# Performance work log

Measured on AMD Instinct MI355X. Metric: run time of the kernel, lower is better.

## Reference

```python
import jax, jax.numpy as jnp
import numpy as np

B, J, HID, INTER, NL = 4096, 16, 128, 64, 4
NEG = -9.0e15
EDGES = [(0,1),(1,2),(2,3),(0,4),(4,5),(5,6),(0,7),(7,8),(8,9),(8,10),(10,11),(11,12),(8,13),(13,14),(14,15)]
GROUPED = [0,7,1,4,2,5,3,6,8,10,9,13,11,14,12,15]  # flattened nodes_group


def _adjacency_nonzeros():
    A = np.zeros((J, J), np.float32)
    for i, j in EDGES:
        A[i, j] = 1.0
        A[j, i] = 1.0
    A += np.eye(J, dtype=np.float32)
    rows, cols = np.nonzero(A)  # row-major, matches torch adj[mask] = e fill order
    return rows.astype(np.int32), cols.astype(np.int32)


def setup_inputs() -> dict:
    key = jax.random.key(0)
    ks = iter(jax.random.split(key, 64))
    rn = lambda shape, s: jax.random.normal(next(ks), shape, jnp.float32) * s
    rows, cols = _adjacency_nonzeros()
    nnz = rows.shape[0]  # 46
    inp = dict(
        x=jax.random.normal(next(ks), (B, J, 2), jnp.float32),
        # input SemGraphConv (2 -> HID) + its BatchNorm
        gc_in_W=rn((2, 2, HID), 0.7), gc_in_e=1.0 + rn((nnz,), 0.3), gc_in_b=rn((HID,), 0.05),
        bn_in_g=1.0 + rn((HID,), 0.05), bn_in_b=rn((HID,), 0.05),
        # 4 residual blocks x 2 graph convs (HID -> HID)
        W_res=rn((2 * NL, 2, HID, HID), 0.08), e_res=1.0 + rn((2 * NL, nnz), 0.3),
        b_res=rn((2 * NL, HID), 0.05),
        bng_res=1.0 + rn((2 * NL, HID), 0.05), bnb_res=rn((2 * NL, HID), 0.05),
        # 5 GraphNonLocal blocks (1 after input + 1 per residual block)
        nl_g_w=rn((NL + 1, INTER, HID), 0.08), nl_g_b=rn((NL + 1, INTER), 0.05),
        nl_t_w=rn((NL + 1, INTER, HID), 0.08), nl_t_b=rn((NL + 1, INTER), 0.05),
        nl_p_w=rn((NL + 1, INTER, HID), 0.08), nl_p_b=rn((NL + 1, INTER), 0.05),
        nl_cp_w=rn((NL + 1, 2 * INTER), 0.08),  # concat_project 1x1 conv, no bias
        nl_W_w=rn((NL + 1, HID, INTER), 0.08), nl_W_b=rn((NL + 1, HID), 0.05),
        nl_bn_g=1.0 + rn((NL + 1, HID), 0.05), nl_bn_b=rn((NL + 1, HID), 0.05),
        # output SemGraphConv (HID -> 3)
        gc_out_W=rn((2, HID, 3), 0.08), gc_out_e=1.0 + rn((nnz,), 0.3), gc_out_b=rn((3,), 0.05),
        # integer constants
        mask_rows=jnp.asarray(rows), mask_cols=jnp.asarray(cols),
        grouped_order=jnp.asarray(GROUPED, jnp.int32),
        restored_order=jnp.asarray(np.argsort(GROUPED), jnp.int32),
    )
    return inp


def reference(x, gc_in_W, gc_in_e, gc_in_b, bn_in_g, bn_in_b,
              W_res, e_res, b_res, bng_res, bnb_res,
              nl_g_w, nl_g_b, nl_t_w, nl_t_b, nl_p_w, nl_p_b,
              nl_cp_w, nl_W_w, nl_W_b, nl_bn_g, nl_bn_b,
              gc_out_W, gc_out_e, gc_out_b,
              mask_rows, mask_cols, grouped_order, restored_order):
    eye = jnp.eye(J, dtype=x.dtype)

    def gconv(h, W, e, b):
        # h: [B, J, F]
        h0 = jnp.einsum('bjf,fo->bjo', h, W[0])
        h1 = jnp.einsum('bjf,fo->bjo', h, W[1])
        logits = jnp.full((J, J), NEG, h.dtype).at[mask_rows, mask_cols].set(e)
        adj = jax.nn.softmax(logits, axis=1)
        diag = jnp.diagonal(adj)                     # adj*I picks diagonal scaling
        off = adj * (1.0 - eye)
        return diag[None, :, None] * h0 + jnp.einsum('ij,bjo->bio', off, h1) + b

    def bn(h, g, bta, axes):
        # training-mode BatchNorm (biased variance), per-channel
        m = h.mean(axes, keepdims=True)
        v = h.var(axes, keepdims=True)
        return (h - m) * jax.lax.rsqrt(v + 1e-5) * g + bta

    def graph_conv(h, W, e, b, gm, gb):
        h = gconv(h, W, e, b)
        h = bn(h, gm[None, None, :], gb[None, None, :], (0, 1))
        return jax.nn.relu(h)

    def nonlocal_block(h, i):
        xo = h[:, grouped_order]          # [B, J, C] regroup joints
        xc = xo.transpose(0, 2, 1)        # [B, C, J]
        conv = lambda w, bb: jnp.einsum('oc,bcj->boj', w, xc) + bb[None, :, None]
        pool = lambda t: t.reshape(B, INTER, J // 2, 2).max(-1)   # MaxPool1d(k=2)
        gx = pool(conv(nl_g_w[i], nl_g_b[i]))                     # [B, I, J/2]
        th = conv(nl_t_w[i], nl_t_b[i])                           # [B, I, J]
        ph = pool(conv(nl_p_w[i], nl_p_b[i]))                     # [B, I, J/2]
        wt, wp = nl_cp_w[i][:INTER], nl_cp_w[i][INTER:]
        # concat_project 1x1 conv over concat(theta,phi) decomposes into a sum
        f = jax.nn.relu(jnp.einsum('bch,c->bh', th, wt)[:, :, None]
                        + jnp.einsum('bcw,c->bw', ph, wp)[:, None, :])  # [B, J, J/2]
        f = f / (J // 2)
        y = jnp.einsum('bhw,bcw->bch', f, gx)                     # [B, I, J]
        Wy = jnp.einsum('oc,bch->boh', nl_W_w[i], y) + nl_W_b[i][None, :, None]
        Wy = bn(Wy, nl_bn_g[i][None, :, None], nl_bn_b[i][None, :, None], (0, 2))
        z = Wy + xc
        return z.transpose(0, 2, 1)[:, restored_order]

    out = graph_conv(x, gc_in_W, gc_in_e, gc_in_b, bn_in_g, bn_in_b)
    out = nonlocal_block(out, 0)
    for i in range(NL):
        res = out
        out = graph_conv(out, W_res[2 * i], e_res[2 * i], b_res[2 * i], bng_res[2 * i], bnb_res[2 * i])
        out = graph_conv(out, W_res[2 * i + 1], e_res[2 * i + 1], b_res[2 * i + 1], bng_res[2 * i + 1], bnb_res[2 * i + 1])
        out = res + out
        out = nonlocal_block(out, i + 1)
    return gconv(out, gc_out_W, gc_out_e, gc_out_b)  # [B, J, 3]
```

## Files before the change

kernel.cpp:

```cpp
#include <hip/hip_runtime.h>

#define B 4096
#define J 16
#define HID 128
#define INTER 64
#define NLAYERS 4
#define NEGV -9000000000000000.0f
#define ELEMS ((size_t)B*16*128)
#define NREP 16
#define SLOT 4096

typedef __attribute__((ext_vector_type(8))) short short8;
typedef __attribute__((ext_vector_type(4))) float f32x4;

static __device__ __forceinline__ unsigned short f2bf(float x) {
    unsigned u = __float_as_uint(x);
    unsigned r = u + 0x7fffu + ((u >> 16) & 1u);
    return (unsigned short)(r >> 16);
}
static __device__ __forceinline__ void splitbf(float x, unsigned short& h, unsigned short& l) {
    h = f2bf(x);
    float hf = __uint_as_float((unsigned)h << 16);
    l = f2bf(x - hf);
}
static __device__ __forceinline__ void splitbf4(float4 v, uint2& hh, uint2& ll) {
    unsigned short h0,l0,h1,l1,h2,l2,h3,l3;
    splitbf(v.x,h0,l0); splitbf(v.y,h1,l1); splitbf(v.z,h2,l2); splitbf(v.w,h3,l3);
    hh = make_uint2((unsigned)h0 | ((unsigned)h1<<16), (unsigned)h2 | ((unsigned)h3<<16));
    ll = make_uint2((unsigned)l0 | ((unsigned)l1<<16), (unsigned)l2 | ((unsigned)l3<<16));
}
static __device__ __forceinline__ f32x4 mfma16(short8 a, short8 b, f32x4 c) {
    return __builtin_amdgcn_mfma_f32_16x16x32_bf16(a, b, c, 0, 0, 0);
}
static __device__ __forceinline__ f32x4 mfma_split(short8 ah, short8 al,
                                                   short8 bh, short8 bl, f32x4 acc) {
    acc = mfma16(ah, bh, acc);
    acc = mfma16(ah, bl, acc);
    acc = mfma16(al, bh, acc);
    return acc;
}
static __device__ __forceinline__ float bfpair(unsigned short h, unsigned short l) {
    return __uint_as_float((unsigned)h << 16) + __uint_as_float((unsigned)l << 16);
}

__global__ void adj_kernel(const float* __restrict__ e_in,
                           const float* __restrict__ e_res,
                           const float* __restrict__ e_out,
                           const int* __restrict__ rows,
                           const int* __restrict__ cols, int nnz,
                           float* __restrict__ off_all,
                           float* __restrict__ diag_all) {
    int m = blockIdx.x;
    int i = threadIdx.x;
    const float* e = (m == 0) ? e_in : (m <= 8) ? e_res + (size_t)(m - 1) * nnz : e_out;
    float l[16];
    for (int j = 0; j < 16; j++) l[j] = NEGV;
    for (int k = 0; k < nnz; k++)
        if (rows[k] == i) l[cols[k]] = e[k];
    float mx = l[0];
    for (int j = 1; j < 16; j++) mx = fmaxf(mx, l[j]);
    float ex[16], s = 0.f;
    for (int j = 0; j < 16; j++) { ex[j] = expf(l[j] - mx); s += ex[j]; }
    float inv = 1.f / s;
    for (int j = 0; j < 16; j++) {
        float a = ex[j] * inv;
        if (j == i) { diag_all[m * 16 + i] = a; a = 0.f; }
        off_all[m * 256 + i * 16 + j] = a;
    }
}

#define WB_N   262144
#define NLW_N  122880
#define NLWW_N 40960
__global__ void prep_w_kernel(const float* __restrict__ W_res,
                              const float* __restrict__ g_w, const float* __restrict__ t_w,
                              const float* __restrict__ p_w, const float* __restrict__ W_w,
                              unsigned short* __restrict__ Wbh, unsigned short* __restrict__ Wbl,
                              unsigned short* __restrict__ nlwh, unsigned short* __restrict__ nlwl,
                              unsigned short* __restrict__ nlWh, unsigned short* __restrict__ nlWl) {
    int i = blockIdx.x * 256 + threadIdx.x;
    unsigned short h, l;
    if (i < WB_N) {
        int lay = i >> 15, rem = i & 32767, n = rem >> 8, k = rem & 255;
        int d = k >> 7, f = k & 127;
        splitbf(W_res[(((lay << 1) | d) * 128 + f) * 128 + n], h, l);
        Wbh[i] = h; Wbl[i] = l;
    } else if (i < WB_N + NLW_N) {
        int j = i - WB_N;
        int lay = j / 24576, r2 = j % 24576;
        int conv = r2 >> 13, oc = r2 & 8191;
        const float* src = conv == 0 ? g_w : conv == 1 ? t_w : p_w;
        splitbf(src[lay * 8192 + oc], h, l);
        nlwh[j] = h; nlwl[j] = l;
    } else if (i < WB_N + NLW_N + NLWW_N) {
        int j = i - WB_N - NLW_N;
        splitbf(W_w[j], h, l);
        nlWh[j] = h; nlWl[j] = l;
    }
}

__global__ void prep_vt_kernel(const float* __restrict__ t_w, const float* __restrict__ t_b,
                               const float* __restrict__ cp_w,
                               float* __restrict__ vt, float* __restrict__ ct) {
    int l = blockIdx.x, c = threadIdx.x;
    float s = 0.f;
    for (int c2 = 0; c2 < 64; c2++)
        s += cp_w[l * 128 + c2] * t_w[(l * 64 + c2) * 128 + c];
    vt[l * 128 + c] = s;
    if (c == 0) {
        float s2 = 0.f;
        for (int c2 = 0; c2 < 64; c2++) s2 += cp_w[l * 128 + c2] * t_b[l * 64 + c2];
        ct[l] = s2;
    }
}

__global__ __launch_bounds__(256) void gconv_in_kernel(
        const float* __restrict__ x, const float* __restrict__ W,
        const float* __restrict__ bias, const float* __restrict__ off,
        const float* __restrict__ diag, float* __restrict__ out,
        float* __restrict__ stats_out) {
    __shared__ float xs[16][2];
    __shared__ float gs[16][2];
    __shared__ float red[512];
    int b = blockIdx.x, t = threadIdx.x;
    if (t < 32) xs[t >> 1][t & 1] = x[b * 32 + t];
    __syncthreads();
    if (t < 32) {
        int i = t >> 1, f = t & 1;
        float g = 0.f;
        #pragma unroll
        for (int j = 0; j < 16; j++) g += off[i * 16 + j] * xs[j][f];
        gs[i][f] = g;
    }
    __syncthreads();
    int o = t & 127;
    float w00 = W[o], w01 = W[128 + o], w10 = W[256 + o], w11 = W[384 + o], bo = bias[o];
    float s = 0.f, q = 0.f;
    for (int idx = t; idx < 2048; idx += 256) {
        int i = idx >> 7;
        float v = diag[i] * (xs[i][0] * w00 + xs[i][1] * w01)
                + gs[i][0] * w10 + gs[i][1] * w11 + bo;
        out[(size_t)b * 2048 + idx] = v;
        s += v; q += v * v;
    }
    red[t] = s; red[256 + t] = q;
    __syncthreads();
    float* so = stats_out + (b & (NREP - 1)) * 256;
    if (t < 128) {
        atomicAdd(&so[t], red[t] + red[t + 128]);
        atomicAdd(&so[128 + t], red[256 + t] + red[256 + t + 128]);
    }
}

__global__ __launch_bounds__(256) void gconv_mfma_kernel(
        const float* src, const float* wy,
        const float* __restrict__ stats_in,
        const float* __restrict__ bn_g, const float* __restrict__ bn_b,
        const int* __restrict__ restored, float* zdst,
        const unsigned short* __restrict__ Wbh,
        const unsigned short* __restrict__ Wbl,
        const float* __restrict__ bias,
        const float* __restrict__ off, const float* __restrict__ diag,
        float* dst, float* __restrict__ stats_out) {
    __shared__ float hraw[16][132];
    __shared__ __align__(16) unsigned short ksh[16][264];
    __shared__ __align__(16) unsigned short ksl[16][264];
    __shared__ float offs[256];
    __shared__ float diags[16];
    int t = threadIdx.x;
    offs[t] = off[t];
    if (t < 16) diags[t] = diag[t];
    float* hrawf = &hraw[0][0];
    {
        float ssum = 0.f;
        #pragma unroll
        for (int rr = 0; rr < NREP; rr++) ssum += stats_in[rr * 256 + t];
        hrawf[t] = ssum;
    }
    int c4 = (4 * t) & 127;
    int r0 = t >> 5;
    int ro0 = 0, ro1 = 0;
    if (wy) { ro0 = restored[r0]; ro1 = restored[r0 + 8]; }
    int b0 = blockIdx.x;
    const float4* src4 = (const float4*)src;
    const float4* wy4  = (const float4*)wy;
    float4 sv0 = src4[(size_t)b0 * 512 + t];
    float4 sv1 = src4[(size_t)b0 * 512 + 256 + t];
    float4 wv0 = make_float4(0,0,0,0), wv1 = make_float4(0,0,0,0);
    if (wy) {
        wv0 = wy4[(size_t)b0 * 512 + ro0 * 32 + (c4 >> 2)];
        wv1 = wy4[(size_t)b0 * 512 + ro1 * 32 + (c4 >> 2)];
    }
    __syncthreads();
    float4 m4, sc4, bb4;
    {
        const float K = 1.f / 65536.f;
        float4 g4 = *(const float4*)&bn_g[c4];
        bb4 = *(const float4*)&bn_b[c4];
        float m0 = hrawf[c4]     * K, m1 = hrawf[c4 + 1] * K;
        float m2 = hrawf[c4 + 2] * K, m3 = hrawf[c4 + 3] * K;
        float i0 = rsqrtf(hrawf[128 + c4]     * K - m0 * m0 + 1e-5f);
        float i1 = rsqrtf(hrawf[128 + c4 + 1] * K - m1 * m1 + 1e-5f);
        float i2 = rsqrtf(hrawf[128 + c4 + 2] * K - m2 * m2 + 1e-5f);
        float i3 = rsqrtf(hrawf[128 + c4 + 3] * K - m3 * m3 + 1e-5f);
        m4 = make_float4(m0, m1, m2, m3);
        sc4 = make_float4(i0 * g4.x, i1 * g4.y, i2 * g4.z, i3 * g4.w);
    }
    __syncthreads();
    int wv_ = t >> 6, lane = t & 63;
    int mn = lane & 15, kq = (lane >> 4) << 3, qr = (lane >> 4) << 2;

    for (int s = 0; s < 2; s++) {
        int bb_ = blockIdx.x + s * 2048;
        {
            float4 v = sv0;
            if (wy) {
                v.x += (wv0.x - m4.x) * sc4.x + bb4.x;
                v.y += (wv0.y - m4.y) * sc4.y + bb4.y;
                v.z += (wv0.z - m4.z) * sc4.z + bb4.z;
                v.w += (wv0.w - m4.w) * sc4.w + bb4.w;
                ((float4*)zdst)[(size_t)bb_ * 512 + t] = v;
            } else {
                v.x = fmaxf((v.x - m4.x) * sc4.x + bb4.x, 0.f);
                v.y = fmaxf((v.y - m4.y) * sc4.y + bb4.y, 0.f);
                v.z = fmaxf((v.z - m4.z) * sc4.z + bb4.z, 0.f);
                v.w = fmaxf((v.w - m4.w) * sc4.w + bb4.w, 0.f);
            }
            *(float4*)&hraw[r0][c4] = v;
            v = sv1;
            if (wy) {
                v.x += (wv1.x - m4.x) * sc4.x + bb4.x;
                v.y += (wv1.y - m4.y) * sc4.y + bb4.y;
                v.z += (wv1.z - m4.z) * sc4.z + bb4.z;
                v.w += (wv1.w - m4.w) * sc4.w + bb4.w;
                ((float4*)zdst)[(size_t)bb_ * 512 + 256 + t] = v;
            } else {
                v.x = fmaxf((v.x - m4.x) * sc4.x + bb4.x, 0.f);
                v.y = fmaxf((v.y - m4.y) * sc4.y + bb4.y, 0.f);
                v.z = fmaxf((v.z - m4.z) * sc4.z + bb4.z, 0.f);
                v.w = fmaxf((v.w - m4.w) * sc4.w + bb4.w, 0.f);
            }
            *(float4*)&hraw[r0 + 8][c4] = v;
        }
        if (s == 0) {
            int b1 = blockIdx.x + 2048;
            sv0 = src4[(size_t)b1 * 512 + t];
            sv1 = src4[(size_t)b1 * 512 + 256 + t];
            if (wy) {
                wv0 = wy4[(size_t)b1 * 512 + ro0 * 32 + (c4 >> 2)];
                wv1 = wy4[(size_t)b1 * 512 + ro1 * 32 + (c4 >> 2)];
            }
        }
        __syncthreads();
        for (int u = t; u < 512; u += 256) {
            int i = u >> 5, f4 = (u & 31) << 2;
            float4 hv = *(const float4*)&hraw[i][f4];
            float4 g = make_float4(0.f, 0.f, 0.f, 0.f);
            #pragma unroll
            for (int j = 0; j < 16; j++) {
                float w = offs[i * 16 + j];
                float4 hj = *(const float4*)&hraw[j][f4];
                g.x += w * hj.x; g.y += w * hj.y; g.z += w * hj.z; g.w += w * hj.w;
            }
            float d = diags[i];
            uint2 hh, ll;
            splitbf4(make_float4(d * hv.x, d * hv.y, d * hv.z, d * hv.w), hh, ll);
            *(uint2*)&ksh[i][f4] = hh;
            *(uint2*)&ksl[i][f4] = ll;
            splitbf4(g, hh, ll);
            *(uint2*)&ksh[i][128 + f4] = hh;
            *(uint2*)&ksl[i][128 + f4] = ll;
        }
        __syncthreads();
        int n0 = wv_ << 5;
        f32x4 acc0 = {0.f, 0.f, 0.f, 0.f}, acc1 = {0.f, 0.f, 0.f, 0.f};
        const unsigned short* wh0 = Wbh + (size_t)(n0 + mn) * 256 + kq;
        const unsigned short* wl0 = Wbl + (size_t)(n0 + mn) * 256 + kq;
        #pragma unroll
        for (int k = 0; k < 8; k++) {
            int k0 = k << 5;
            short8 ah = *(const short8*)&ksh[mn][k0 + kq];
            short8 al = *(const short8*)&ksl[mn][k0 + kq];
            acc0 = mfma_split(ah, al, *(const short8*)(wh0 + k0), *(const short8*)(wl0 + k0), acc0);
            acc1 = mfma_split(ah, al, *(const short8*)(wh0 + 4096 + k0), *(const short8*)(wl0 + 4096 + k0), acc1);
        }
        float bias0 = bias[n0 + mn], bias1 = bias[n0 + 16 + mn];
        float s0 = 0.f, q0 = 0.f, s1 = 0.f, q1 = 0.f;
        #pragma unroll
        for (int r = 0; r < 4; r++) {
            int row = qr + r;
            float v0 = acc0[r] + bias0;
            float v1 = acc1[r] + bias1;
            dst[(size_t)bb_ * 2048 + row * 128 + n0 + mn] = v0;
            dst[(size_t)bb_ * 2048 + row * 128 + n0 + 16 + mn] = v1;
            s0 += v0; q0 += v0 * v0; s1 += v1; q1 += v1 * v1;
        }
        s0 += __shfl_xor(s0, 16); s0 += __shfl_xor(s0, 32);
        q0 += __shfl_xor(q0, 16); q0 += __shfl_xor(q0, 32);
        s1 += __shfl_xor(s1, 16); s1 += __shfl_xor(s1, 32);
        q1 += __shfl_xor(q1, 16); q1 += __shfl_xor(q1, 32);
        float* so = stats_out + (bb_ & (NREP - 1)) * 256;
        if (lane < 16) {
            atomicAdd(&so[n0 + mn], s0);
            atomicAdd(&so[128 + n0 + mn], q0);
            atomicAdd(&so[n0 + 16 + mn], s1);
            atomicAdd(&so[128 + n0 + 16 + mn], q1);
        }
        if (s == 0) __syncthreads();
    }
}

#define CG(conv, o, j) cgbuf[((conv) * 64 + (o)) * 17 + (j)]
#define WYL(o, j)      cgbuf[(o) * 17 + (j)]
__global__ __launch_bounds__(512, 8) void nl_a_kernel(
        const float* tsrc, const float* __restrict__ stats_in,
        const float* __restrict__ bn_g, const float* __restrict__ bn_b,
        const float* res,
        const unsigned short* __restrict__ nlwh,
        const unsigned short* __restrict__ nlwl,
        const float* __restrict__ g_b, const float* __restrict__ p_b,
        const float* __restrict__ cpw,
        const float* __restrict__ vt, const float* __restrict__ ctp,
        const unsigned short* __restrict__ nlWh,
        const unsigned short* __restrict__ nlWl,
        const float* __restrict__ W_b,
        const int* __restrict__ restored,
        float* hdst, float* wydst, float* __restrict__ wst) {
    __shared__ __align__(16) unsigned short xch[16][136];
    __shared__ __align__(16) unsigned short xcl[16][136];
    __shared__ float cgbuf[2176];
    __shared__ float gx[64][9];
    __shared__ float tv[16], pv[8];
    __shared__ float vtl[128];
    __shared__ __align__(16) float bnm[128], bnsc[128], bnbb[128];
    __shared__ __align__(16) unsigned short ybh[16][72];
    __shared__ __align__(16) unsigned short ybl[16][72];
    __shared__ float redS[512], redQ[512];
    int t = threadIdx.x, b = blockIdx.x;
    const float4* tsrc4 = (const float4*)tsrc;
    float4 sv = tsrc4[(size_t)b * 512 + t];
    float4 rv = make_float4(0.f, 0.f, 0.f, 0.f);
    if (res) rv = ((const float4*)res)[(size_t)b * 512 + t];
    if (t < 256) {
        float ssum = 0.f;
        #pragma unroll
        for (int rr = 0; rr < NREP; rr++) ssum += stats_in[rr * 256 + t];
        redS[t] = ssum;
    }
    if (t < 128) vtl[t] = vt[t];
    int c4 = (4 * t) & 127;
    int r0 = t >> 5;
    int rg = restored[r0];
    __syncthreads();
    if (t < 128) {
        const float K = 1.f / 65536.f;
        float mean = redS[t] * K;
        float varv = redS[128 + t] * K - mean * mean;
        bnm[t] = mean;
        bnsc[t] = rsqrtf(varv + 1e-5f) * bn_g[t];
        bnbb[t] = bn_b[t];
    }
    __syncthreads();
    int w = t >> 6, lane = t & 63;
    int mn = lane & 15, kq = (lane >> 4) << 3, qr = (lane >> 4) << 2;
    {
        float4 m4 = *(const float4*)&bnm[c4];
        float4 sc4 = *(const float4*)&bnsc[c4];
        float4 bb4 = *(const float4*)&bnbb[c4];
        float4 v;
        v.x = fmaxf((sv.x - m4.x) * sc4.x + bb4.x, 0.f) + rv.x;
        v.y = fmaxf((sv.y - m4.y) * sc4.y + bb4.y, 0.f) + rv.y;
        v.z = fmaxf((sv.z - m4.z) * sc4.z + bb4.z, 0.f) + rv.z;
        v.w = fmaxf((sv.w - m4.w) * sc4.w + bb4.w, 0.f) + rv.w;
        ((float4*)hdst)[(size_t)b * 512 + t] = v;
        uint2 hh, ll;
        splitbf4(v, hh, ll);
        *(uint2*)&xch[rg][c4] = hh;
        *(uint2*)&xcl[rg][c4] = ll;
    }
    __syncthreads();
    {
        int conv = w >> 2;
        int mt = w & 3;
        int wbase = (conv == 0) ? 0 : 128;
        const unsigned short* aph = nlwh + (size_t)(wbase + mt * 16 + mn) * 128 + kq;
        const unsigned short* apl = nlwl + (size_t)(wbase + mt * 16 + mn) * 128 + kq;
        f32x4 acc = {0.f, 0.f, 0.f, 0.f};
        #pragma unroll
        for (int k = 0; k < 4; k++) {
            short8 bh = *(const short8*)&xch[mn][k * 32 + kq];
            short8 bl = *(const short8*)&xcl[mn][k * 32 + kq];
            acc = mfma_split(*(const short8*)(aph + k * 32), *(const short8*)(apl + k * 32),
                             bh, bl, acc);
        }
        const float* biasp = (conv == 0) ? g_b : p_b;
        #pragma unroll
        for (int r = 0; r < 4; r++) {
            int o = mt * 16 + qr + r;
            CG(conv, o, mn) = acc[r] + biasp[o];
        }
    }
    __syncthreads();
    {
        int c = t >> 3, w2 = t & 7;
        gx[c][w2] = fmaxf(CG(0, c, 2 * w2), CG(0, c, 2 * w2 + 1));
        if (t < 64) {
            int ch = t >> 3;
            float ss = 0.f;
            for (int cc = ch * 8; cc < ch * 8 + 8; cc++)
                ss += fmaxf(CG(1, cc, 2 * w2), CG(1, cc, 2 * w2 + 1)) * cpw[64 + cc];
            ss += __shfl_xor(ss, 8);
            ss += __shfl_xor(ss, 16);
            ss += __shfl_xor(ss, 32);
            if (t < 8) pv[t] = ss;
        } else if (t < 128) {
            int u = t - 64, j = u & 15, ch = u >> 4;
            float ss = 0.f;
            int c0 = ch * 32;
            for (int cc = c0; cc < c0 + 32; cc += 2) {
                unsigned hh = *(const unsigned*)&xch[j][cc];
                unsigned ll = *(const unsigned*)&xcl[j][cc];
                float v0 = bfpair((unsigned short)hh, (unsigned short)ll);
                float v1 = bfpair((unsigned short)(hh >> 16), (unsigned short)(ll >> 16));
                ss += vtl[cc] * v0 + vtl[cc + 1] * v1;
            }
            ss += __shfl_xor(ss, 16);
            ss += __shfl_xor(ss, 32);
            if (u < 16) tv[u] = ss + ctp[0];
        }
    }
    __syncthreads();
    #pragma unroll
    for (int u2 = 0; u2 < 2; u2++) {
        int u = t + u2 * 512;
        int j = u >> 6, c = u & 63;
        float ss = 0.f;
        #pragma unroll
        for (int w2 = 0; w2 < 8; w2++)
            ss += fmaxf(tv[j] + pv[w2], 0.f) * gx[c][w2];
        unsigned short h2, l2;
        splitbf(ss * 0.125f, h2, l2);
        ybh[j][c] = h2; ybl[j][c] = l2;
    }
    __syncthreads();
    {
        int mt = w;
        short8 byh0 = *(const short8*)&ybh[mn][kq];
        short8 byh1 = *(const short8*)&ybh[mn][32 + kq];
        short8 byl0 = *(const short8*)&ybl[mn][kq];
        short8 byl1 = *(const short8*)&ybl[mn][32 + kq];
        const unsigned short* aph = nlWh + (size_t)(mt * 16 + mn) * 64 + kq;
        const unsigned short* apl = nlWl + (size_t)(mt * 16 + mn) * 64 + kq;
        f32x4 acc = {0.f, 0.f, 0.f, 0.f};
        acc = mfma_split(*(const short8*)aph, *(const short8*)apl, byh0, byl0, acc);
        acc = mfma_split(*(const short8*)(aph + 32), *(const short8*)(apl + 32), byh1, byl1, acc);
        #pragma unroll
        for (int r = 0; r < 4; r++) {
            int o = mt * 16 + qr + r;
            WYL(o, mn) = acc[r] + W_b[o];
        }
    }
    __syncthreads();
    {
        int c = t & 127;
        float ss = 0.f, qq = 0.f;
        #pragma unroll
        for (int u2 = 0; u2 < 4; u2++) {
            int idx = t + u2 * 512;
            int j = idx >> 7;
            float v = WYL(c, j);
            wydst[(size_t)b * 2048 + idx] = v;
            ss += v; qq += v * v;
        }
        redS[t] = ss; redQ[t] = qq;
        __syncthreads();
        float* so = wst + (b & (NREP - 1)) * 256;
        if (t < 128) {
            float s4 = redS[t] + redS[t + 128] + redS[t + 256] + redS[t + 384];
            float q4 = redQ[t] + redQ[t + 128] + redQ[t + 256] + redQ[t + 384];
            atomicAdd(&so[t], s4);
            atomicAdd(&so[128 + t], q4);
        }
    }
}

__global__ __launch_bounds__(256) void gconv_out_kernel(
        const float* __restrict__ h, const float* __restrict__ wy,
        const float* __restrict__ stats_in,
        const float* __restrict__ nlg, const float* __restrict__ nlb,
        const int* __restrict__ restored,
        const float* __restrict__ W,
        const float* __restrict__ bias, const float* __restrict__ off,
        const float* __restrict__ diag, float* __restrict__ out) {
    __shared__ float hs[16][132];
    __shared__ float gsv[16][132];
    __shared__ float offs[256];
    __shared__ float p0[48][4], p1[48][4];
    int b = blockIdx.x, t = threadIdx.x;
    offs[t] = off[t];
    float* hsf = &hs[0][0];
    {
        float ssum = 0.f;
        #pragma unroll
        for (int rr = 0; rr < NREP; rr++) ssum += stats_in[rr * 256 + t];
        hsf[t] = ssum;
    }
    __syncthreads();
    int c = t & 127;
    float mean, inv, bbv;
    {
        const float K = 1.f / 65536.f;
        mean = hsf[c] * K;
        float varv = hsf[128 + c] * K - mean * mean;
        inv = rsqrtf(varv + 1e-5f) * nlg[c];
        bbv = nlb[c];
    }
    __syncthreads();
    {
        for (int idx = t; idx < 2048; idx += 256) {
            int r = idx >> 7;
            float wval = wy[(size_t)b * 2048 + restored[r] * 128 + c];
            hs[r][c] = (wval - mean) * inv + bbv + h[(size_t)b * 2048 + idx];
        }
    }
    __syncthreads();
    for (int idx = t; idx < 2048; idx += 256) {
        int i = idx >> 7, f = idx & 127;
        float g = 0.f;
        #pragma unroll
        for (int j = 0; j < 16; j++) g += offs[i * 16 + j] * hs[j][f];
        gsv[i][f] = g;
    }
    __syncthreads();
    if (t < 192) {
        int oid = t >> 2, chunk = t & 3;
        int i = oid / 3, o = oid % 3;
        float a0 = 0.f, a1 = 0.f;
        int f0 = chunk * 32;
        for (int f = f0; f < f0 + 32; f++) {
            a0 += hs[i][f] * W[f * 3 + o];
            a1 += gsv[i][f] * W[384 + f * 3 + o];
        }
        p0[oid][chunk] = a0; p1[oid][chunk] = a1;
    }
    __syncthreads();
    if (t < 48) {
        int i = t / 3, o = t % 3;
        float a0 = p0[t][0] + p0[t][1] + p0[t][2] + p0[t][3];
        float a1 = p1[t][0] + p1[t][1] + p1[t][2] + p1[t][3];
        out[(size_t)b * 48 + t] = diag[i] * a0 + a1 + bias[o];
    }
}

extern "C" void kernel_launch(void* const* d_in, const int* in_sizes, int n_in,
                              void* d_out, int out_size, void* d_ws, size_t ws_size,
                              hipStream_t stream) {
    (void)n_in; (void)out_size; (void)ws_size;
    const float* x        = (const float*)d_in[0];
    const float* gc_in_W  = (const float*)d_in[1];
    const float* gc_in_e  = (const float*)d_in[2];
    const float* gc_in_b  = (const float*)d_in[3];
    const float* bn_in_g  = (const float*)d_in[4];
    const float* bn_in_b  = (const float*)d_in[5];
    const float* W_res    = (const float*)d_in[6];
    const float* e_res    = (const float*)d_in[7];
    const float* b_res    = (const float*)d_in[8];
    const float* bng_res  = (const float*)d_in[9];
    const float* bnb_res  = (const float*)d_in[10];
    const float* nl_g_w   = (const float*)d_in[11];
    const float* nl_g_b   = (const float*)d_in[12];
    const float* nl_t_w   = (const float*)d_in[13];
    const float* nl_t_b   = (const float*)d_in[14];
    const float* nl_p_w   = (const float*)d_in[15];
    const float* nl_p_b   = (const float*)d_in[16];
    const float* nl_cp_w  = (const float*)d_in[17];
    const float* nl_W_w   = (const float*)d_in[18];
    const float* nl_W_b   = (const float*)d_in[19];
    const float* nl_bn_g  = (const float*)d_in[20];
    const float* nl_bn_b  = (const float*)d_in[21];
    const float* gc_out_W = (const float*)d_in[22];
    const float* gc_out_e = (const float*)d_in[23];
    const float* gc_out_b = (const float*)d_in[24];
    const int*   mask_rows = (const int*)d_in[25];
    const int*   mask_cols = (const int*)d_in[26];
    const int*   restored  = (const int*)d_in[28];
    int nnz = in_sizes[2];

    float* ws       = (float*)d_ws;
    float* off_all  = ws;
    float* diag_all = ws + 2560;
    float* stats    = ws + 2720;
    float* vt       = ws + 63664;
    float* ct       = ws + 64304;
    unsigned short* Wbh  = (unsigned short*)(ws + 65536);
    unsigned short* Wbl  = Wbh + WB_N;
    unsigned short* nlwh = Wbl + WB_N;
    unsigned short* nlwl = nlwh + NLW_N;
    unsigned short* nlWh = nlwl + NLW_N;
    unsigned short* nlWl = nlWh + NLWW_N;
    float* Z = ws + 491520;
    float* T = Z + ELEMS;

    hipMemsetAsync(stats, 0, 14 * SLOT * sizeof(float), stream);
    adj_kernel<<<10, 16, 0, stream>>>(gc_in_e, e_res, gc_out_e, mask_rows, mask_cols,
                                      nnz, off_all, diag_all);
    prep_w_kernel<<<(WB_N + NLW_N + NLWW_N + 255) / 256, 256, 0, stream>>>(
        W_res, nl_g_w, nl_t_w, nl_p_w, nl_W_w, Wbh, Wbl, nlwh, nlwl, nlWh, nlWl);
    prep_vt_kernel<<<5, 128, 0, stream>>>(nl_t_w, nl_t_b, nl_cp_w, vt, ct);

    gconv_in_kernel<<<B, 256, 0, stream>>>(x, gc_in_W, gc_in_b, off_all, diag_all,
                                           T, stats);
    nl_a_kernel<<<B, 512, 0, stream>>>(T, stats, bn_in_g, bn_in_b, nullptr,
                                       nlwh, nlwl, nl_g_b, nl_p_b, nl_cp_w,
                                       vt, ct, nlWh, nlWl, nl_W_b, restored,
                                       Z, T, stats + SLOT);

    int sl = 1;
    for (int i = 0; i < NLAYERS; i++) {
        int l0 = 2 * i, l1 = 2 * i + 1, li = i + 1;
        gconv_mfma_kernel<<<2048, 256, 0, stream>>>(
            Z, T, stats + (size_t)sl * SLOT,
            nl_bn_g + i * 128, nl_bn_b + i * 128, restored, Z,
            Wbh + (size_t)l0 * 32768, Wbl + (size_t)l0 * 32768, b_res + l0 * 128,
            off_all + (1 + l0) * 256, diag_all + (1 + l0) * 16, T,
            stats + (size_t)(sl + 1) * SLOT);
        gconv_mfma_kernel<<<2048, 256, 0, stream>>>(
            T, nullptr, stats + (size_t)(sl + 1) * SLOT,
            bng_res + l0 * 128, bnb_res + l0 * 128, nullptr, nullptr,
            Wbh + (size_t)l1 * 32768, Wbl + (size_t)l1 * 32768, b_res + l1 * 128,
            off_all + (1 + l1) * 256, diag_all + (1 + l1) * 16, T,
            stats + (size_t)(sl + 2) * SLOT);
        nl_a_kernel<<<B, 512, 0, stream>>>(
            T, stats + (size_t)(sl + 2) * SLOT,
            bng_res + l1 * 128, bnb_res + l1 * 128, Z,
            nlwh + li * 24576, nlwl + li * 24576,
            nl_g_b + li * 64, nl_p_b + li * 64, nl_cp_w + li * 128,
            vt + li * 128, ct + li, nlWh + li * 8192, nlWl + li * 8192,
            nl_W_b + li * 128, restored, Z, T,
            stats + (size_t)(sl + 3) * SLOT);
        sl += 3;
    }
    gconv_out_kernel<<<B, 256, 0, stream>>>(Z, T, stats + (size_t)sl * SLOT,
                                            nl_bn_g + NLAYERS * 128, nl_bn_b + NLAYERS * 128,
                                            restored, gc_out_W, gc_out_b,
                                            off_all + 9 * 256, diag_all + 9 * 16,
                                            (float*)d_out);
}
```

Baseline: 889.0 us.

## Halve nl_a_kernel block size, reuse shared buffers, drop BN staging and reductions

Reworks the non-local block kernel to run with 256 threads instead of 512, so each thread handles two rows and each wave computes two MFMA tiles. The BN scale and shift are now computed in registers straight from the reduced stats, which drops the bnm/bnsc/bnbb shared arrays and one barrier. The y buffers alias the xch/xcl shared arrays, and the final stats reduction uses per-thread atomics in place of a shared-memory tree. The hdst store is deferred to the end of the kernel. The goal is lower LDS use and fewer barriers so more blocks fit per CU, at the cost of more work per thread and twice as many global atomics.

```diff
diff --git a/kernel.cpp b/kernel.cpp
--- a/kernel.cpp
+++ b/kernel.cpp
@@ -312,7 +312,7 @@
 
 #define CG(conv, o, j) cgbuf[((conv) * 64 + (o)) * 17 + (j)]
 #define WYL(o, j)      cgbuf[(o) * 17 + (j)]
-__global__ __launch_bounds__(512, 8) void nl_a_kernel(
+__global__ __launch_bounds__(256, 8) void nl_a_kernel(
         const float* tsrc, const float* __restrict__ stats_in,
         const float* __restrict__ bn_g, const float* __restrict__ bn_b,
         const float* res,
@@ -332,16 +332,19 @@
     __shared__ float gx[64][9];
     __shared__ float tv[16], pv[8];
     __shared__ float vtl[128];
-    __shared__ __align__(16) float bnm[128], bnsc[128], bnbb[128];
-    __shared__ __align__(16) unsigned short ybh[16][72];
-    __shared__ __align__(16) unsigned short ybl[16][72];
-    __shared__ float redS[512], redQ[512];
+    __shared__ float redS[256];
+    unsigned short (*ybh)[72] = (unsigned short (*)[72])&xch[0][0];
+    unsigned short (*ybl)[72] = (unsigned short (*)[72])&xcl[0][0];
     int t = threadIdx.x, b = blockIdx.x;
     const float4* tsrc4 = (const float4*)tsrc;
-    float4 sv = tsrc4[(size_t)b * 512 + t];
-    float4 rv = make_float4(0.f, 0.f, 0.f, 0.f);
-    if (res) rv = ((const float4*)res)[(size_t)b * 512 + t];
-    if (t < 256) {
+    float4 sv0 = tsrc4[(size_t)b * 512 + t];
+    float4 sv1 = tsrc4[(size_t)b * 512 + 256 + t];
+    float4 rv0 = make_float4(0.f, 0.f, 0.f, 0.f), rv1 = rv0;
+    if (res) {
+        rv0 = ((const float4*)res)[(size_t)b * 512 + t];
+        rv1 = ((const float4*)res)[(size_t)b * 512 + 256 + t];
+    }
+    {
         float ssum = 0.f;
         #pragma unroll
         for (int rr = 0; rr < NREP; rr++) ssum += stats_in[rr * 256 + t];
@@ -350,38 +353,44 @@
     if (t < 128) vtl[t] = vt[t];
     int c4 = (4 * t) & 127;
     int r0 = t >> 5;
-    int rg = restored[r0];
-    __syncthreads();
-    if (t < 128) {
-        const float K = 1.f / 65536.f;
-        float mean = redS[t] * K;
-        float varv = redS[128 + t] * K - mean * mean;
-        bnm[t] = mean;
-        bnsc[t] = rsqrtf(varv + 1e-5f) * bn_g[t];
-        bnbb[t] = bn_b[t];
-    }
+    int rg0 = restored[r0];
+    int rg1 = restored[r0 + 8];
     __syncthreads();
     int w = t >> 6, lane = t & 63;
     int mn = lane & 15, kq = (lane >> 4) << 3, qr = (lane >> 4) << 2;
-    {
-        float4 m4 = *(const float4*)&bnm[c4];
-        float4 sc4 = *(const float4*)&bnsc[c4];
-        float4 bb4 = *(const float4*)&bnbb[c4];
-        float4 v;
-        v.x = fmaxf((sv.x - m4.x) * sc4.x + bb4.x, 0.f) + rv.x;
-        v.y = fmaxf((sv.y - m4.y) * sc4.y + bb4.y, 0.f) + rv.y;
-        v.z = fmaxf((sv.z - m4.z) * sc4.z + bb4.z, 0.f) + rv.z;
-        v.w = fmaxf((sv.w - m4.w) * sc4.w + bb4.w, 0.f) + rv.w;
-        ((float4*)hdst)[(size_t)b * 512 + t] = v;
+    float4 h0, h1;
+    {
+        const float K = 1.f / 65536.f;
+        float4 g4 = *(const float4*)&bn_g[c4];
+        float4 bb4 = *(const float4*)&bn_b[c4];
+        float m0 = redS[c4] * K,       m1 = redS[c4 + 1] * K;
+        float m2 = redS[c4 + 2] * K,   m3 = redS[c4 + 3] * K;
+        float s0 = rsqrtf(redS[128 + c4]     * K - m0 * m0 + 1e-5f) * g4.x;
+        float s1 = rsqrtf(redS[128 + c4 + 1] * K - m1 * m1 + 1e-5f) * g4.y;
+        float s2 = rsqrtf(redS[128 + c4 + 2] * K - m2 * m2 + 1e-5f) * g4.z;
+        float s3 = rsqrtf(redS[128 + c4 + 3] * K - m3 * m3 + 1e-5f) * g4.w;
+        h0.x = fmaxf((sv0.x - m0) * s0 + bb4.x, 0.f) + rv0.x;
+        h0.y = fmaxf((sv0.y - m1) * s1 + bb4.y, 0.f) + rv0.y;
+        h0.z = fmaxf((sv0.z - m2) * s2 + bb4.z, 0.f) + rv0.z;
+        h0.w = fmaxf((sv0.w - m3) * s3 + bb4.w, 0.f) + rv0.w;
+        h1.x = fmaxf((sv1.x - m0) * s0 + bb4.x, 0.f) + rv1.x;
+        h1.y = fmaxf((sv1.y - m1) * s1 + bb4.y, 0.f) + rv1.y;
+        h1.z = fmaxf((sv1.z - m2) * s2 + bb4.z, 0.f) + rv1.z;
+        h1.w = fmaxf((sv1.w - m3) * s3 + bb4.w, 0.f) + rv1.w;
         uint2 hh, ll;
-        splitbf4(v, hh, ll);
-        *(uint2*)&xch[rg][c4] = hh;
-        *(uint2*)&xcl[rg][c4] = ll;
-    }
-    __syncthreads();
-    {
-        int conv = w >> 2;
-        int mt = w & 3;
+        splitbf4(h0, hh, ll);
+        *(uint2*)&xch[rg0][c4] = hh;
+        *(uint2*)&xcl[rg0][c4] = ll;
+        splitbf4(h1, hh, ll);
+        *(uint2*)&xch[rg1][c4] = hh;
+        *(uint2*)&xcl[rg1][c4] = ll;
+    }
+    __syncthreads();
+    #pragma unroll
+    for (int i = 0; i < 2; i++) {
+        int tile = 2 * w + i;
+        int conv = tile >> 2;
+        int mt = tile & 3;
         int wbase = (conv == 0) ? 0 : 128;
         const unsigned short* aph = nlwh + (size_t)(wbase + mt * 16 + mn) * 128 + kq;
         const unsigned short* apl = nlwl + (size_t)(wbase + mt * 16 + mn) * 128 + kq;
@@ -402,10 +411,14 @@
     }
     __syncthreads();
     {
-        int c = t >> 3, w2 = t & 7;
-        gx[c][w2] = fmaxf(CG(0, c, 2 * w2), CG(0, c, 2 * w2 + 1));
+        #pragma unroll
+        for (int u2 = 0; u2 < 2; u2++) {
+            int u = t + u2 * 256;
+            int cc = u >> 3, w2 = u & 7;
+            gx[cc][w2] = fmaxf(CG(0, cc, 2 * w2), CG(0, cc, 2 * w2 + 1));
+        }
         if (t < 64) {
-            int ch = t >> 3;
+            int ch = t >> 3, w2 = t & 7;
             float ss = 0.f;
             for (int cc = ch * 8; cc < ch * 8 + 8; cc++)
                 ss += fmaxf(CG(1, cc, 2 * w2), CG(1, cc, 2 * w2 + 1)) * cpw[64 + cc];
@@ -431,8 +444,8 @@
     }
     __syncthreads();
     #pragma unroll
-    for (int u2 = 0; u2 < 2; u2++) {
-        int u = t + u2 * 512;
+    for (int u2 = 0; u2 < 4; u2++) {
+        int u = t + u2 * 256;
         int j = u >> 6, c = u & 63;
         float ss = 0.f;
         #pragma unroll
@@ -444,20 +457,23 @@
     }
     __syncthreads();
     {
-        int mt = w;
         short8 byh0 = *(const short8*)&ybh[mn][kq];
         short8 byh1 = *(const short8*)&ybh[mn][32 + kq];
         short8 byl0 = *(const short8*)&ybl[mn][kq];
         short8 byl1 = *(const short8*)&ybl[mn][32 + kq];
-        const unsigned short* aph = nlWh + (size_t)(mt * 16 + mn) * 64 + kq;
-        const unsigned short* apl = nlWl + (size_t)(mt * 16 + mn) * 64 + kq;
-        f32x4 acc = {0.f, 0.f, 0.f, 0.f};
-        acc = mfma_split(*(const short8*)aph, *(const short8*)apl, byh0, byl0, acc);
-        acc = mfma_split(*(const short8*)(aph + 32), *(const short8*)(apl + 32), byh1, byl1, acc);
-        #pragma unroll
-        for (int r = 0; r < 4; r++) {
-            int o = mt * 16 + qr + r;
-            WYL(o, mn) = acc[r] + W_b[o];
+        #pragma unroll
+        for (int i = 0; i < 2; i++) {
+            int mt = 2 * w + i;
+            const unsigned short* aph = nlWh + (size_t)(mt * 16 + mn) * 64 + kq;
+            const unsigned short* apl = nlWl + (size_t)(mt * 16 + mn) * 64 + kq;
+            f32x4 acc = {0.f, 0.f, 0.f, 0.f};
+            acc = mfma_split(*(const short8*)aph, *(const short8*)apl, byh0, byl0, acc);
+            acc = mfma_split(*(const short8*)(aph + 32), *(const short8*)(apl + 32), byh1, byl1, acc);
+            #pragma unroll
+            for (int r = 0; r < 4; r++) {
+                int o = mt * 16 + qr + r;
+                WYL(o, mn) = acc[r] + W_b[o];
+            }
         }
     }
     __syncthreads();
@@ -465,22 +481,18 @@
         int c = t & 127;
         float ss = 0.f, qq = 0.f;
         #pragma unroll
-        for (int u2 = 0; u2 < 4; u2++) {
-            int idx = t + u2 * 512;
+        for (int u2 = 0; u2 < 8; u2++) {
+            int idx = t + u2 * 256;
             int j = idx >> 7;
             float v = WYL(c, j);
             wydst[(size_t)b * 2048 + idx] = v;
             ss += v; qq += v * v;
         }
-        redS[t] = ss; redQ[t] = qq;
-        __syncthreads();
         float* so = wst + (b & (NREP - 1)) * 256;
-        if (t < 128) {
-            float s4 = redS[t] + redS[t + 128] + redS[t + 256] + redS[t + 384];
-            float q4 = redQ[t] + redQ[t + 128] + redQ[t + 256] + redQ[t + 384];
-            atomicAdd(&so[t], s4);
-            atomicAdd(&so[128 + t], q4);
-        }
+        atomicAdd(&so[c], ss);
+        atomicAdd(&so[128 + c], qq);
+        ((float4*)hdst)[(size_t)b * 512 + t] = h0;
+        ((float4*)hdst)[(size_t)b * 512 + 256 + t] = h1;
     }
 }
 
@@ -610,7 +622,7 @@
 
     gconv_in_kernel<<<B, 256, 0, stream>>>(x, gc_in_W, gc_in_b, off_all, diag_all,
                                            T, stats);
-    nl_a_kernel<<<B, 512, 0, stream>>>(T, stats, bn_in_g, bn_in_b, nullptr,
+    nl_a_kernel<<<B, 256, 0, stream>>>(T, stats, bn_in_g, bn_in_b, nullptr,
                                        nlwh, nlwl, nl_g_b, nl_p_b, nl_cp_w,
                                        vt, ct, nlWh, nlWl, nl_W_b, restored,
                                        Z, T, stats + SLOT);
@@ -630,7 +642,7 @@
             Wbh + (size_t)l1 * 32768, Wbl + (size_t)l1 * 32768, b_res + l1 * 128,
             off_all + (1 + l1) * 256, diag_all + (1 + l1) * 16, T,
             stats + (size_t)(sl + 2) * SLOT);
-        nl_a_kernel<<<B, 512, 0, stream>>>(
+        nl_a_kernel<<<B, 256, 0, stream>>>(
             T, stats + (size_t)(sl + 2) * SLOT,
             bng_res + l1 * 128, bnb_res + l1 * 128, Z,
             nlwh + li * 24576, nlwl + li * 24576,
```

Result: no change. 893.2 us (+0.5%).
